# Performance work log

Hardware: AMD Instinct MI355X
Metric: run time of the kernel (lower is better)

The kernel has to match this reference:

```python
import jax, jax.numpy as jnp
import numpy as np

B, S, E = 2, 2048, 1024
H, HD = 16, 64
ROPE, NOPE = 32, 32          # qk_rope_head_dim, head_dim - rope
QL, KVL = 512, 512           # q_lora_rank, kv_lora_rank
EPS = 1e-5


def _layernorm(u, g, b):
    mu = jnp.mean(u, axis=-1, keepdims=True)
    var = jnp.mean(jnp.square(u - mu), axis=-1, keepdims=True)
    return (u - mu) * jax.lax.rsqrt(var + EPS) * g + b


def _rope_tables(seq_len):
    inv_freq = 1.0 / (10000.0 ** (jnp.arange(0, ROPE, 2, dtype=jnp.float32) / ROPE))
    freqs = jnp.arange(seq_len, dtype=jnp.float32)[:, None] * inv_freq[None, :]  # [S, ROPE/2]
    return jnp.cos(freqs), jnp.sin(freqs)


def _apply_rope(t, cos, sin):
    # t: [B, H, S, ROPE]; cos/sin: [S, ROPE/2]
    x1, x2 = t[..., ::2], t[..., 1::2]
    c = cos[None, None, :, :]
    s = sin[None, None, :, :]
    r1 = x1 * c - x2 * s
    r2 = x1 * s + x2 * c
    return jnp.stack([r1, r2], axis=-1).reshape(t.shape)  # interleave back


def setup_inputs() -> dict:
    key = jax.random.key(0)
    ks = jax.random.split(key, 8)
    w = 0.02
    return {
        "x": jax.random.normal(ks[0], (B, S, E), dtype=jnp.float32),
        "Wqa": jax.random.normal(ks[1], (QL, E), dtype=jnp.float32) * w,
        "g_qa": jnp.ones((QL,), jnp.float32),
        "b_qa": jnp.zeros((QL,), jnp.float32),
        "Wqb": jax.random.normal(ks[2], (H * HD, QL), dtype=jnp.float32) * w,
        "Wkva": jax.random.normal(ks[3], (KVL + ROPE, E), dtype=jnp.float32) * w,
        "g_kva": jnp.ones((KVL,), jnp.float32),
        "b_kva": jnp.zeros((KVL,), jnp.float32),
        "Wkvb": jax.random.normal(ks[4], (H * (NOPE + HD), KVL), dtype=jnp.float32) * w,
        "Wout": jax.random.normal(ks[5], (E, H * HD), dtype=jnp.float32) * w,
    }


def reference(x, Wqa, g_qa, b_qa, Wqb, Wkva, g_kva, b_kva, Wkvb, Wout):
    # --- query path: low-rank compress -> LN -> decompress ---
    qc = _layernorm(jnp.einsum('bse,re->bsr', x, Wqa), g_qa, b_qa)      # [B,S,QL]
    q = jnp.einsum('bsr,dr->bsd', qc, Wqb).reshape(B, S, H, HD)
    q = q.transpose(0, 2, 1, 3)                                          # [B,H,S,HD]
    q_nope, q_pe = q[..., :NOPE], q[..., NOPE:]

    # --- kv path: joint compress with decoupled rope part ---
    kva = jnp.einsum('bse,re->bsr', x, Wkva)                             # [B,S,KVL+ROPE]
    ckv, k_pe = kva[..., :KVL], kva[..., KVL:]
    ckv = _layernorm(ckv, g_kva, b_kva)
    kvd = jnp.einsum('bsr,dr->bsd', ckv, Wkvb).reshape(B, S, H, NOPE + HD)
    kvd = kvd.transpose(0, 2, 1, 3)                                       # [B,H,S,NOPE+HD]
    k_nope, v = kvd[..., :NOPE], kvd[..., NOPE:]
    k_pe = k_pe[:, None, :, :]                                            # [B,1,S,ROPE]

    # --- decoupled RoPE ---
    cos, sin = _rope_tables(S)
    q_pe = _apply_rope(q_pe, cos, sin)
    k_pe = jnp.broadcast_to(_apply_rope(k_pe, cos, sin), (B, H, S, ROPE))

    q_full = jnp.concatenate([q_nope, q_pe], axis=-1)                     # [B,H,S,HD]
    k_full = jnp.concatenate([k_nope, k_pe], axis=-1)

    scale = 1.0 / np.sqrt(HD).astype(np.float32)
    scores = jnp.einsum('bhsd,bhtd->bhst', q_full, k_full) * scale        # [B,H,S,S]
    attn = jax.nn.softmax(scores, axis=-1)
    out = jnp.einsum('bhst,bhtd->bhsd', attn, v)                          # [B,H,S,HD]
    out = out.transpose(0, 2, 1, 3).reshape(B, S, H * HD)
    return jnp.einsum('bsd,ed->bse', out, Wout)
```

## Files before the change

kernel.cpp:

```cpp
#include <hip/hip_runtime.h>
#include <math.h>

#define B_SZ 2
#define S_SZ 2048
#define E_SZ 1024
#define H_SZ 16
#define HD_SZ 64

#define ATT_SCALE 0.1803368801111306f
#define ROPE_L2 0.8304820237218407f

typedef unsigned short u16;
typedef unsigned int u32;
typedef __bf16 bf16_t;
typedef bf16_t bf16x8 __attribute__((ext_vector_type(8)));
typedef float f32x4 __attribute__((ext_vector_type(4)));

__device__ __forceinline__ u16 f2bf(float f) {
    bf16_t h = (bf16_t)f;
    union { bf16_t h; u16 u; } v; v.h = h;
    return v.u;
}

__device__ __forceinline__ void gload_lds16(const void* g, void* l) {
    __builtin_amdgcn_global_load_lds(
        (const __attribute__((address_space(1))) unsigned int*)g,
        (__attribute__((address_space(3))) unsigned int*)l, 16, 0, 0);
}

#define N_X   4194304L
#define N_QA  524288L
#define N_QB  524288L
#define N_KVA 557056L
#define N_KVB 786432L

__global__ __launch_bounds__(256) void init_kernel(
    const float* __restrict__ x, const float* __restrict__ wqa,
    const float* __restrict__ wqb, const float* __restrict__ wkva,
    const float* __restrict__ wkvb, const float* __restrict__ wout,
    u16* __restrict__ xb, u16* __restrict__ wqab, u16* __restrict__ wqbb,
    u16* __restrict__ wkvab, u16* __restrict__ wkvbb, u16* __restrict__ woutb,
    float2* __restrict__ tbl)
{
    if (blockIdx.x < 128) {
        const int idx = blockIdx.x * 256 + threadIdx.x;
        const int s = idx >> 4, i = idx & 15;
        const float invf = exp2f(-(float)i * ROPE_L2);
        float sn, c;
        sincosf((float)s * invf, &sn, &c);
        tbl[idx] = make_float2(c, sn);
        return;
    }
    long i = ((long)(blockIdx.x - 128) * 256 + threadIdx.x) * 8;
    const long c0 = N_X, c1 = c0 + N_QA, c2 = c1 + N_QB, c3 = c2 + N_KVA, c4 = c3 + N_KVB;
    const float* src; u16* dst; long off;
    if      (i < c0) { src = x;    dst = xb;    off = i; }
    else if (i < c1) { src = wqa;  dst = wqab;  off = i - c0; }
    else if (i < c2) { src = wqb;  dst = wqbb;  off = i - c1; }
    else if (i < c3) { src = wkva; dst = wkvab; off = i - c2; }
    else if (i < c4) { src = wkvb; dst = wkvbb; off = i - c3; }
    else             { src = wout; dst = woutb; off = i - c4; }
    float v[8];
    *(float4*)v       = *(const float4*)(src + off);
    *(float4*)(v + 4) = *(const float4*)(src + off + 4);
    u32 o[4];
    #pragma unroll
    for (int k = 0; k < 4; ++k)
        o[k] = (u32)f2bf(v[2*k]) | ((u32)f2bf(v[2*k+1]) << 16);
    *(uint4*)(dst + off) = *(const uint4*)o;
}

template<bool BF16OUT>
__device__ __forceinline__ void gemm_body(
    const u16* __restrict__ A, int lda,
    const u16* __restrict__ Bm, int ldb,
    void* __restrict__ Cout, int ldc, int N, int K,
    int m0, int n0, u16* smA, u16* smB)
{
    const int tid = threadIdx.x;
    const int wave = tid >> 6, lane = tid & 63;
    const int wm = wave >> 1, wn = wave & 1;

    f32x4 acc[4][4] = {};
    const int rA0 = wm * 64 + (lane & 15);
    const int rB0 = wn * 64 + (lane & 15);
    const int cfr = lane >> 4;

    for (int k0 = 0; k0 < K; k0 += 32) {
        #pragma unroll
        for (int j = 0; j < 2; ++j) {
            const int boff = j * 4096 + wave * 1024;
            const int r  = (boff >> 6) + (lane >> 2);
            const int ch = lane & 3;
            const int sw = (ch ^ ((r >> 1) & 3)) * 8;
            gload_lds16(A + (size_t)(m0 + r) * lda + k0 + sw, (char*)smA + boff);
            const int nr = min(n0 + r, N - 1);
            gload_lds16(Bm + (size_t)nr * ldb + k0 + sw, (char*)smB + boff);
        }
        __syncthreads();
        bf16x8 af[4], bfr[4];
        #pragma unroll
        for (int f = 0; f < 4; ++f) {
            const int rA = rA0 + f * 16;
            af[f]  = *(const bf16x8*)(smA + rA * 32 + ((cfr ^ ((rA >> 1) & 3)) * 8));
            const int rB = rB0 + f * 16;
            bfr[f] = *(const bf16x8*)(smB + rB * 32 + ((cfr ^ ((rB >> 1) & 3)) * 8));
        }
        #pragma unroll
        for (int i = 0; i < 4; ++i)
            #pragma unroll
            for (int j = 0; j < 4; ++j)
                acc[i][j] = __builtin_amdgcn_mfma_f32_16x16x32_bf16(af[i], bfr[j], acc[i][j], 0, 0, 0);
        __syncthreads();
    }

    const int cn = lane & 15, rq = lane >> 4;
    #pragma unroll
    for (int i = 0; i < 4; ++i) {
        #pragma unroll
        for (int j = 0; j < 4; ++j) {
            const int n = n0 + wn * 64 + j * 16 + cn;
            if (n < N) {
                #pragma unroll
                for (int r = 0; r < 4; ++r) {
                    const size_t row = (size_t)(m0 + wm * 64 + i * 16 + rq * 4 + r);
                    if (BF16OUT) ((u16*)Cout)[row * ldc + n] = f2bf(acc[i][j][r]);
                    else         ((float*)Cout)[row * ldc + n] = acc[i][j][r];
                }
            }
        }
    }
}

__device__ __forceinline__ int swz_bid() {
    const int nx = gridDim.x;
    const int bid = blockIdx.x + nx * blockIdx.y;
    const int cpx = (nx * gridDim.y) >> 3;
    return (bid & 7) * cpx + (bid >> 3);
}

template<bool BF16OUT>
__global__ __launch_bounds__(256) void gemm_bt_bf16(
    const u16* __restrict__ A, int lda,
    const u16* __restrict__ Bm, int ldb,
    void* __restrict__ Cout, int ldc, int N, int K)
{
    __shared__ u16 smA[128 * 32];
    __shared__ u16 smB[128 * 32];
    const int w = swz_bid();
    const int nx = gridDim.x;
    gemm_body<BF16OUT>(A, lda, Bm, ldb, Cout, ldc, N, K,
                       (w / nx) * 128, (w % nx) * 128, smA, smB);
}

__global__ __launch_bounds__(256) void gemm_dual(
    const u16* __restrict__ A,
    const u16* __restrict__ B1, float* __restrict__ C1,
    const u16* __restrict__ B2, float* __restrict__ C2)
{
    __shared__ u16 smA[128 * 32];
    __shared__ u16 smB[128 * 32];
    const int w = swz_bid();
    const int bx = w % 9, by = w / 9;
    if (bx < 4)
        gemm_body<false>(A, 1024, B1, 1024, C1, 512, 512, 1024,
                         by * 128, bx * 128, smA, smB);
    else
        gemm_body<false>(A, 1024, B2, 1024, C2, 544, 544, 1024,
                         by * 128, (bx - 4) * 128, smA, smB);
}

__global__ __launch_bounds__(256) void gemm_qkv(
    const u16* __restrict__ qcb, const u16* __restrict__ wqbb,
    const u16* __restrict__ ckvb, const u16* __restrict__ wkvbb,
    const float2* __restrict__ tbl,
    u16* __restrict__ qpack, u16* __restrict__ kvd_b)
{
    __shared__ u16 smA[128 * 32];
    __shared__ u16 smB[128 * 32];
    const int tid = threadIdx.x;
    const int wave = tid >> 6, lane = tid & 63;
    const int wm = wave >> 1, wn = wave & 1;
    const int wsw = swz_bid();
    const int bx = wsw % 20, by = wsw / 20;
    const bool qpath = bx < 8;
    const u16* A  = qpath ? qcb : ckvb;
    const u16* Bm = qpath ? wqbb : wkvbb;
    const int n0 = (qpath ? bx : bx - 8) * 128;
    const int m0 = by * 128;

    f32x4 acc[4][4] = {};
    const int rA0 = wm * 64 + (lane & 15);
    const int rB0 = wn * 64 + (lane & 15);
    const int cfr = lane >> 4;

    for (int k0 = 0; k0 < 512; k0 += 32) {
        #pragma unroll
        for (int j = 0; j < 2; ++j) {
            const int boff = j * 4096 + wave * 1024;
            const int r  = (boff >> 6) + (lane >> 2);
            const int ch = lane & 3;
            const int sw = (ch ^ ((r >> 1) & 3)) * 8;
            gload_lds16(A + (size_t)(m0 + r) * 512 + k0 + sw, (char*)smA + boff);
            gload_lds16(Bm + (size_t)(n0 + r) * 512 + k0 + sw, (char*)smB + boff);
        }
        __syncthreads();
        bf16x8 af[4], bfr[4];
        #pragma unroll
        for (int f = 0; f < 4; ++f) {
            const int rA = rA0 + f * 16;
            af[f]  = *(const bf16x8*)(smA + rA * 32 + ((cfr ^ ((rA >> 1) & 3)) * 8));
            const int rB = rB0 + f * 16;
            bfr[f] = *(const bf16x8*)(smB + rB * 32 + ((cfr ^ ((rB >> 1) & 3)) * 8));
        }
        #pragma unroll
        for (int i = 0; i < 4; ++i)
            #pragma unroll
            for (int j = 0; j < 4; ++j)
                acc[i][j] = __builtin_amdgcn_mfma_f32_16x16x32_bf16(af[i], bfr[j], acc[i][j], 0, 0, 0);
        __syncthreads();
    }

    const int cn = lane & 15, rq = lane >> 4;
    if (qpath) {
        #pragma unroll
        for (int i = 0; i < 4; ++i) {
            #pragma unroll
            for (int j = 0; j < 4; ++j) {
                const int n = n0 + wn * 64 + j * 16 + cn;
                const int d = n & 63, h = n >> 6;
                #pragma unroll
                for (int r = 0; r < 4; ++r) {
                    const int row = m0 + wm * 64 + i * 16 + rq * 4 + r;
                    const int s = row & (S_SZ - 1), b = row >> 11;
                    const float val = acc[i][j][r];
                    const float prt = __shfl_xor(val, 1);
                    float o;
                    if (d >= 32) {
                        const float2 cs = tbl[s * 16 + ((d - 32) >> 1)];
                        o = (d & 1) ? (prt * cs.y + val * cs.x)
                                    : (val * cs.x - prt * cs.y);
                    } else {
                        o = val;
                    }
                    o *= ATT_SCALE;
                    const int sch = (d >> 3) ^ (s & 7);
                    qpack[(((size_t)(b * 16 + h) * S_SZ + s) * 64) + sch * 8 + (d & 7)] = f2bf(o);
                }
            }
        }
    } else {
        #pragma unroll
        for (int i = 0; i < 4; ++i) {
            #pragma unroll
            for (int j = 0; j < 4; ++j) {
                const int n = n0 + wn * 64 + j * 16 + cn;
                #pragma unroll
                for (int r = 0; r < 4; ++r) {
                    const size_t row = (size_t)(m0 + wm * 64 + i * 16 + rq * 4 + r);
                    kvd_b[row * 1536 + n] = f2bf(acc[i][j][r]);
                }
            }
        }
    }
}

__global__ __launch_bounds__(256) void ln2_kernel(
    const float* __restrict__ qc, const float* __restrict__ kva,
    const float* __restrict__ g_qa, const float* __restrict__ b_qa,
    const float* __restrict__ g_kva, const float* __restrict__ b_kva,
    u16* __restrict__ qcb, u16* __restrict__ ckvb,
    float* __restrict__ kpe, const float2* __restrict__ tbl)
{
    const bool qpart = blockIdx.x < 4096;
    const int row = blockIdx.x & 4095;
    const float* in    = qpart ? qc : kva;
    const int ld       = qpart ? 512 : 544;
    const float* gamma = qpart ? g_qa : g_kva;
    const float* beta  = qpart ? b_qa : b_kva;
    u16* outb          = qpart ? qcb : ckvb;

    const float* p = in + (size_t)row * ld;
    const int t = threadIdx.x;
    float v0 = p[t], v1 = p[t + 256];

    __shared__ float red[4];
    const int wave = t >> 6, lane = t & 63;

    float s = v0 + v1;
    #pragma unroll
    for (int o = 1; o < 64; o <<= 1) s += __shfl_xor(s, o);
    if (lane == 0) red[wave] = s;
    __syncthreads();
    const float mu = (red[0] + red[1] + red[2] + red[3]) * (1.f / 512.f);

    const float d0 = v0 - mu, d1 = v1 - mu;
    float s2 = d0 * d0 + d1 * d1;
    #pragma unroll
    for (int o = 1; o < 64; o <<= 1) s2 += __shfl_xor(s2, o);
    __syncthreads();
    if (lane == 0) red[wave] = s2;
    __syncthreads();
    const float var = (red[0] + red[1] + red[2] + red[3]) * (1.f / 512.f);
    const float rs = rsqrtf(var + 1e-5f);

    outb[(size_t)row * 512 + t]       = f2bf(d0 * rs * gamma[t]       + beta[t]);
    outb[(size_t)row * 512 + t + 256] = f2bf(d1 * rs * gamma[t + 256] + beta[t + 256]);

    if (!qpart && t < 16) {
        const int spos = row & (S_SZ - 1);
        const float2 cs = tbl[spos * 16 + t];
        const float x1 = p[512 + 2*t], x2 = p[512 + 2*t + 1];
        kpe[(size_t)row * 32 + 2*t]     = x1 * cs.x - x2 * cs.y;
        kpe[(size_t)row * 32 + 2*t + 1] = x1 * cs.y + x2 * cs.x;
    }
}

__device__ __forceinline__ int pi_v(int s) {
    return ((s >> 5) << 5) | ((((s >> 2) & 1)) << 4) | ((((s >> 3) & 3)) << 2) | (s & 3);
}

__global__ __launch_bounds__(256) void pack_kv_kernel(
    const u16* __restrict__ kvd_b, const float* __restrict__ kpe,
    u16* __restrict__ kpack, u16* __restrict__ vt)
{
    __shared__ u16 tr[64 * 74];
    const int t = threadIdx.x;
    if (blockIdx.x < 2048) {
        const int idx = blockIdx.x * 256 + t;
        const int p = idx & 7, h = (idx >> 3) & 15, row = idx >> 7;
        const int s = row & (S_SZ - 1), b = row >> 11;
        u32 o[4];
        if (p < 4) {
            const u16* src = kvd_b + (size_t)row * 1536 + h * 96 + p * 8;
            *(uint4*)o = *(const uint4*)src;
        } else {
            const float* src = kpe + (size_t)row * 32 + (p - 4) * 8;
            float v[8];
            *(float4*)v       = *(const float4*)(src);
            *(float4*)(v + 4) = *(const float4*)(src + 4);
            #pragma unroll
            for (int k = 0; k < 4; ++k)
                o[k] = (u32)f2bf(v[2*k]) | ((u32)f2bf(v[2*k+1]) << 16);
        }
        const int sch = p ^ (s & 7);
        *(uint4*)(kpack + (((size_t)(b * 16 + h) * S_SZ + s) * 64) + sch * 8) = *(const uint4*)o;
        return;
    }
    const int v = blockIdx.x - 2048;
    const int kt = v & 31, h = (v >> 5) & 15, b = v >> 9;
    {
        const int kc = t >> 2, dp = t & 3;
        const u16* src = kvd_b + (size_t)(b * S_SZ + kt * 64 + kc) * 1536 + h * 96 + 32 + dp * 16;
        u16 vals[16];
        *(uint4*)vals       = *(const uint4*)src;
        *(uint4*)(vals + 8) = *(const uint4*)(src + 8);
        #pragma unroll
        for (int e = 0; e < 16; ++e) tr[(dp * 16 + e) * 74 + kc] = vals[e];
    }
    __syncthreads();
    {
        const int d = t >> 2, kp = t & 3;
        u16 o[16];
        #pragma unroll
        for (int e = 0; e < 16; ++e) o[e] = tr[d * 74 + pi_v(kp * 16 + e)];
        const size_t obase = (((size_t)(b * 16 + h) * (S_SZ / 64) + kt) * 64 + d) * 64;
        const int c0 = (kp * 2)     ^ (d & 7);
        const int c1 = (kp * 2 + 1) ^ (d & 7);
        *(uint4*)(vt + obase + c0 * 8) = *(const uint4*)o;
        *(uint4*)(vt + obase + c1 * 8) = *(const uint4*)(o + 8);
    }
}

__global__ __launch_bounds__(256) void attn_mfma_kernel(
    const u16* __restrict__ qpack, const u16* __restrict__ kpack,
    const u16* __restrict__ vt, u16* __restrict__ attout)
{
    __shared__ u16 KV[2][2][64 * 64];

    const int bid = blockIdx.x;
    const int w0 = (bid & 7) * 64 + (bid >> 3);
    const int qt = w0 & 15, h = (w0 >> 4) & 15, b = w0 >> 8;
    const int bh = b * H_SZ + h;
    const int tid = threadIdx.x, wave = tid >> 6, lane = tid & 63;
    const int g = lane >> 4, q15 = lane & 15;

    const u16* kbase = kpack + (size_t)bh * S_SZ * 64;
    const u16* vbase = vt + (size_t)bh * (S_SZ / 64) * 4096;

    bf16x8 qa[2][2];
    {
        const u16* qbase = qpack + ((size_t)bh * S_SZ + qt * 128) * 64;
        #pragma unroll
        for (int qb = 0; qb < 2; ++qb) {
            const int r = wave * 32 + qb * 16 + q15;
            #pragma unroll
            for (int dh = 0; dh < 2; ++dh) {
                const int ch = dh * 4 + g;
                qa[qb][dh] = *(const bf16x8*)(qbase + r * 64 + ((ch ^ (r & 7)) * 8));
            }
        }
    }

    int koff[4][2], voff[2][4];
    #pragma unroll
    for (int fk = 0; fk < 4; ++fk) {
        const int kc = fk * 16 + q15;
        #pragma unroll
        for (int dh = 0; dh < 2; ++dh)
            koff[fk][dh] = kc * 128 + (((dh * 4 + g) ^ (kc & 7)) * 16);
    }
    #pragma unroll
    for (int kh = 0; kh < 2; ++kh)
        #pragma unroll
        for (int fd = 0; fd < 4; ++fd) {
            const int d = fd * 16 + q15;
            voff[kh][fd] = 8192 + d * 128 + (((kh * 4 + g) ^ (d & 7)) * 16);
        }

    #pragma unroll
    for (int j = 0; j < 2; ++j) {
        const int boff = j * 4096 + wave * 1024;
        gload_lds16(kbase + boff / 2 + lane * 8, (char*)&KV[0][0][0] + boff);
        gload_lds16(vbase + boff / 2 + lane * 8, (char*)&KV[0][1][0] + boff);
    }
    __syncthreads();

    bf16x8 ones;
    #pragma unroll
    for (int e = 0; e < 8; ++e) ones[e] = (bf16_t)1.0f;

    f32x4 acc[2][4] = {};
    f32x4 acc_l[2] = {};

    #pragma unroll 2
    for (int kt = 0; kt < S_SZ / 64; ++kt) {
        const char* base = (const char*)&KV[kt & 1][0][0];
        char* nbase = (char*)&KV[(kt + 1) & 1][0][0];

        {
            const int ktn = (kt + 1) & 31;
            const u16* kn = kbase + (size_t)ktn * 4096;
            const u16* vn = vbase + (size_t)ktn * 4096;
            #pragma unroll
            for (int j = 0; j < 2; ++j) {
                const int boff = j * 4096 + wave * 1024;
                gload_lds16(kn + boff / 2 + lane * 8, nbase + boff);
                gload_lds16(vn + boff / 2 + lane * 8, nbase + 8192 + boff);
            }
        }

        bf16x8 kb[4][2];
        #pragma unroll
        for (int fk = 0; fk < 4; ++fk)
            #pragma unroll
            for (int dh = 0; dh < 2; ++dh)
                kb[fk][dh] = *(const bf16x8*)(base + koff[fk][dh]);

        f32x4 sc[2][4] = {};
        __builtin_amdgcn_s_setprio(1);
        #pragma unroll
        for (int qb = 0; qb < 2; ++qb)
            #pragma unroll
            for (int fk = 0; fk < 4; ++fk)
                #pragma unroll
                for (int dh = 0; dh < 2; ++dh)
                    sc[qb][fk] = __builtin_amdgcn_mfma_f32_16x16x32_bf16(kb[fk][dh], qa[qb][dh], sc[qb][fk], 0, 0, 0);
        __builtin_amdgcn_s_setprio(0);

        #pragma unroll
        for (int qb = 0; qb < 2; ++qb)
            #pragma unroll
            for (int fk = 0; fk < 4; ++fk)
                #pragma unroll
                for (int r = 0; r < 4; ++r)
                    sc[qb][fk][r] = exp2f(sc[qb][fk][r]);

        bf16x8 pa[2][2];
        #pragma unroll
        for (int qb = 0; qb < 2; ++qb)
            #pragma unroll
            for (int kh = 0; kh < 2; ++kh)
                #pragma unroll
                for (int e = 0; e < 4; ++e) {
                    pa[qb][kh][e]     = (bf16_t)sc[qb][2*kh][e];
                    pa[qb][kh][e + 4] = (bf16_t)sc[qb][2*kh + 1][e];
                }

        bf16x8 vb[2][4];
        #pragma unroll
        for (int kh = 0; kh < 2; ++kh)
            #pragma unroll
            for (int fd = 0; fd < 4; ++fd)
                vb[kh][fd] = *(const bf16x8*)(base + voff[kh][fd]);

        __builtin_amdgcn_s_setprio(1);
        #pragma unroll
        for (int kh = 0; kh < 2; ++kh)
            #pragma unroll
            for (int qb = 0; qb < 2; ++qb) {
                #pragma unroll
                for (int fd = 0; fd < 4; ++fd)
                    acc[qb][fd] = __builtin_amdgcn_mfma_f32_16x16x32_bf16(vb[kh][fd], pa[qb][kh], acc[qb][fd], 0, 0, 0);
                acc_l[qb] = __builtin_amdgcn_mfma_f32_16x16x32_bf16(ones, pa[qb][kh], acc_l[qb], 0, 0, 0);
            }
        __builtin_amdgcn_s_setprio(0);

        __syncthreads();
    }

    #pragma unroll
    for (int qb = 0; qb < 2; ++qb) {
        const float inv = 1.0f / acc_l[qb][0];
        const size_t row = (size_t)(b * S_SZ + qt * 128 + wave * 32 + qb * 16 + q15);
        #pragma unroll
        for (int fd = 0; fd < 4; ++fd) {
            const int d0 = fd * 16 + 4 * g;
            u32 wlo = (u32)f2bf(acc[qb][fd][0] * inv) | ((u32)f2bf(acc[qb][fd][1] * inv) << 16);
            u32 whi = (u32)f2bf(acc[qb][fd][2] * inv) | ((u32)f2bf(acc[qb][fd][3] * inv) << 16);
            *(uint2*)(attout + row * 1024 + h * 64 + d0) = make_uint2(wlo, whi);
        }
    }
}

extern "C" void kernel_launch(void* const* d_in, const int* in_sizes, int n_in,
                              void* d_out, int out_size, void* d_ws, size_t ws_size,
                              hipStream_t stream)
{
    (void)in_sizes; (void)n_in; (void)out_size; (void)ws_size;
    const float* x     = (const float*)d_in[0];
    const float* Wqa   = (const float*)d_in[1];
    const float* g_qa  = (const float*)d_in[2];
    const float* b_qa  = (const float*)d_in[3];
    const float* Wqb   = (const float*)d_in[4];
    const float* Wkva  = (const float*)d_in[5];
    const float* g_kva = (const float*)d_in[6];
    const float* b_kva = (const float*)d_in[7];
    const float* Wkvb  = (const float*)d_in[8];
    const float* Wout  = (const float*)d_in[9];
    float* out = (float*)d_out;

    float* ws = (float*)d_ws;
    u16*   kvd_b   = (u16*)ws;
    u16*   xb      = (u16*)ws;
    float* qc      = ws + 3145728;
    u16*   attout  = (u16*)qc;
    float* kva     = qc + 2097152;
    u16*   qpack   = (u16*)kva;
    u16*   vt      = (u16*)(kva + 2228224 + 2097152);
    float2* tbl    = (float2*)vt;
    float* kpe     = kva + 2228224 + 2097152 + 2097152;
    u16*   qcb     = (u16*)(kpe + 131072);
    u16*   ckvb    = qcb + 2097152;
    u16*   kpack   = ckvb + 2097152;
    u16*   wqab    = kpack + 4194304;
    u16*   wqbb    = wqab + 524288;
    u16*   wkvab   = wqbb + 524288;
    u16*   wkvbb   = wkvab + 557056;
    u16*   woutb   = wkvbb + 786432;

    dim3 blk(256);

    init_kernel<<<3856, blk, 0, stream>>>(x, Wqa, Wqb, Wkva, Wkvb, Wout,
                                          xb, wqab, wqbb, wkvab, wkvbb, woutb, tbl);
    gemm_dual<<<dim3(9, 32), blk, 0, stream>>>(xb, wqab, qc, wkvab, kva);
    ln2_kernel<<<8192, blk, 0, stream>>>(qc, kva, g_qa, b_qa, g_kva, b_kva,
                                         qcb, ckvb, kpe, tbl);
    gemm_qkv<<<dim3(20, 32), blk, 0, stream>>>(qcb, wqbb, ckvb, wkvbb, tbl,
                                               qpack, kvd_b);
    pack_kv_kernel<<<3072, blk, 0, stream>>>(kvd_b, kpe, kpack, vt);
    attn_mfma_kernel<<<dim3(512), blk, 0, stream>>>(qpack, kpack, vt, attout);
    gemm_bt_bf16<false><<<dim3(8, 32), blk, 0, stream>>>(attout, 1024, woutb, 1024, out, 1024, 1024, 1024);
}
```

Baseline: 152.2 us.

## Split attention KV sequence across two wave groups per block with LDS reduction

The attention kernel now runs 512 threads per block. Two groups of four waves each process half of the key/value sequence (16 tiles each), with separate double-buffered LDS regions. The partial outputs and row sums are combined through LDS at the end. Softmax needs no max rescaling here because the kernel already uses unnormalised exp2, so the split-K reduction is a plain sum. This doubles the wave-level parallelism per block, which helps with only 512 blocks on 256 CUs, at the cost of more LDS and an extra reduction pass. The exp2f call is also replaced with the hardware exp2 builtin.

```diff
diff --git a/kernel.cpp b/kernel.cpp
--- a/kernel.cpp
+++ b/kernel.cpp
@@ -372,28 +372,29 @@
     }
 }
 
-__global__ __launch_bounds__(256) void attn_mfma_kernel(
+__global__ __launch_bounds__(512, 4) void attn_mfma_kernel(
     const u16* __restrict__ qpack, const u16* __restrict__ kpack,
     const u16* __restrict__ vt, u16* __restrict__ attout)
 {
-    __shared__ u16 KV[2][2][64 * 64];
+    __shared__ u16 KV[2][2][2][4096];
 
     const int bid = blockIdx.x;
     const int w0 = (bid & 7) * 64 + (bid >> 3);
     const int qt = w0 & 15, h = (w0 >> 4) & 15, b = w0 >> 8;
     const int bh = b * H_SZ + h;
     const int tid = threadIdx.x, wave = tid >> 6, lane = tid & 63;
+    const int kw = wave >> 2, wv = wave & 3;
     const int g = lane >> 4, q15 = lane & 15;
 
-    const u16* kbase = kpack + (size_t)bh * S_SZ * 64;
-    const u16* vbase = vt + (size_t)bh * (S_SZ / 64) * 4096;
+    const u16* kbase = kpack + (size_t)bh * S_SZ * 64 + (size_t)(kw * 16) * 4096;
+    const u16* vbase = vt + (size_t)bh * (S_SZ / 64) * 4096 + (size_t)(kw * 16) * 4096;
 
     bf16x8 qa[2][2];
     {
         const u16* qbase = qpack + ((size_t)bh * S_SZ + qt * 128) * 64;
         #pragma unroll
         for (int qb = 0; qb < 2; ++qb) {
-            const int r = wave * 32 + qb * 16 + q15;
+            const int r = wv * 32 + qb * 16 + q15;
             #pragma unroll
             for (int dh = 0; dh < 2; ++dh) {
                 const int ch = dh * 4 + g;
@@ -420,9 +421,9 @@
 
     #pragma unroll
     for (int j = 0; j < 2; ++j) {
-        const int boff = j * 4096 + wave * 1024;
-        gload_lds16(kbase + boff / 2 + lane * 8, (char*)&KV[0][0][0] + boff);
-        gload_lds16(vbase + boff / 2 + lane * 8, (char*)&KV[0][1][0] + boff);
+        const int boff = j * 4096 + wv * 1024;
+        gload_lds16(kbase + boff / 2 + lane * 8, (char*)&KV[kw][0][0][0] + boff);
+        gload_lds16(vbase + boff / 2 + lane * 8, (char*)&KV[kw][0][1][0] + boff);
     }
     __syncthreads();
 
@@ -434,17 +435,16 @@
     f32x4 acc_l[2] = {};
 
     #pragma unroll 2
-    for (int kt = 0; kt < S_SZ / 64; ++kt) {
-        const char* base = (const char*)&KV[kt & 1][0][0];
-        char* nbase = (char*)&KV[(kt + 1) & 1][0][0];
-
-        {
-            const int ktn = (kt + 1) & 31;
-            const u16* kn = kbase + (size_t)ktn * 4096;
-            const u16* vn = vbase + (size_t)ktn * 4096;
+    for (int t = 0; t < 16; ++t) {
+        const char* base = (const char*)&KV[kw][t & 1][0][0];
+        char* nbase = (char*)&KV[kw][(t + 1) & 1][0][0];
+
+        if (t != 15) {
+            const u16* kn = kbase + (size_t)(t + 1) * 4096;
+            const u16* vn = vbase + (size_t)(t + 1) * 4096;
             #pragma unroll
             for (int j = 0; j < 2; ++j) {
-                const int boff = j * 4096 + wave * 1024;
+                const int boff = j * 4096 + wv * 1024;
                 gload_lds16(kn + boff / 2 + lane * 8, nbase + boff);
                 gload_lds16(vn + boff / 2 + lane * 8, nbase + 8192 + boff);
             }
@@ -474,7 +474,7 @@
             for (int fk = 0; fk < 4; ++fk)
                 #pragma unroll
                 for (int r = 0; r < 4; ++r)
-                    sc[qb][fk][r] = exp2f(sc[qb][fk][r]);
+                    sc[qb][fk][r] = __builtin_amdgcn_exp2f(sc[qb][fk][r]);
 
         bf16x8 pa[2][2];
         #pragma unroll
@@ -509,16 +509,32 @@
         __syncthreads();
     }
 
-    #pragma unroll
-    for (int qb = 0; qb < 2; ++qb) {
-        const float inv = 1.0f / acc_l[qb][0];
-        const size_t row = (size_t)(b * S_SZ + qt * 128 + wave * 32 + qb * 16 + q15);
-        #pragma unroll
-        for (int fd = 0; fd < 4; ++fd) {
-            const int d0 = fd * 16 + 4 * g;
-            u32 wlo = (u32)f2bf(acc[qb][fd][0] * inv) | ((u32)f2bf(acc[qb][fd][1] * inv) << 16);
-            u32 whi = (u32)f2bf(acc[qb][fd][2] * inv) | ((u32)f2bf(acc[qb][fd][3] * inv) << 16);
-            *(uint2*)(attout + row * 1024 + h * 64 + d0) = make_uint2(wlo, whi);
+    float* ex = (float*)&KV[0][0][0][0];
+    const int slot = (wv * 64 + lane) * 36;
+    if (kw == 1) {
+        #pragma unroll
+        for (int qb = 0; qb < 2; ++qb)
+            #pragma unroll
+            for (int fd = 0; fd < 4; ++fd)
+                *(f32x4*)(ex + slot + (qb * 4 + fd) * 4) = acc[qb][fd];
+        ex[slot + 32] = acc_l[0][0];
+        ex[slot + 33] = acc_l[1][0];
+    }
+    __syncthreads();
+    if (kw == 0) {
+        #pragma unroll
+        for (int qb = 0; qb < 2; ++qb) {
+            const float l2 = acc_l[qb][0] + ex[slot + 32 + qb];
+            const float inv = 1.0f / l2;
+            const size_t row = (size_t)(b * S_SZ + qt * 128 + wv * 32 + qb * 16 + q15);
+            #pragma unroll
+            for (int fd = 0; fd < 4; ++fd) {
+                const f32x4 o = acc[qb][fd] + *(const f32x4*)(ex + slot + (qb * 4 + fd) * 4);
+                const int d0 = fd * 16 + 4 * g;
+                u32 wlo = (u32)f2bf(o[0] * inv) | ((u32)f2bf(o[1] * inv) << 16);
+                u32 whi = (u32)f2bf(o[2] * inv) | ((u32)f2bf(o[3] * inv) << 16);
+                *(uint2*)(attout + row * 1024 + h * 64 + d0) = make_uint2(wlo, whi);
+            }
         }
     }
 }
@@ -569,6 +585,6 @@
     gemm_qkv<<<dim3(20, 32), blk, 0, stream>>>(qcb, wqbb, ckvb, wkvbb, tbl,
                                                qpack, kvd_b);
     pack_kv_kernel<<<3072, blk, 0, stream>>>(kvd_b, kpe, kpack, vt);
-    attn_mfma_kernel<<<dim3(512), blk, 0, stream>>>(qpack, kpack, vt, attout);
+    attn_mfma_kernel<<<dim3(512), dim3(512), 0, stream>>>(qpack, kpack, vt, attout);
     gemm_bt_bf16<false><<<dim3(8, 32), blk, 0, stream>>>(attout, 1024, woutb, 1024, out, 1024, 1024, 1024);
 }
```

Result: faster. 136.0 us (-10.7%).
